# Performance work log

Hardware: AMD Instinct MI355X
Metric: run time of the kernel (lower is better)

Reference implementation:

```python
import jax, jax.numpy as jnp
import numpy as np

B, NQ, NC = 256, 15, 30          # pairs, query size, corpus size (= max_set_size)
EQ, EC = 45, 90                  # original directed edges per query / corpus graph
ENEW = NQ * (NC - NQ)            # edges added to pad each query graph
NPG = 2 * NC                     # nodes per pair after padding
N = B * NPG                      # 15360 total nodes
E = B * (EQ + EC + ENEW)         # 92160 total edges
D = 128                          # node_state_dim == filters_3
T = 64                           # transform_dim
N_PROP = 5
SK_ITERS, SK_TEMP = 10, 0.1


def _glorot(rng, shape):
    fan_in, fan_out = shape[0], shape[-1]
    s = np.sqrt(2.0 / (fan_in + fan_out))
    return jnp.asarray(rng.standard_normal(shape) * s, dtype=jnp.float32)


def setup_inputs() -> dict:
    rng = np.random.default_rng(0)
    frs, tos = [], []
    # original edges, grouped per pair as (query graph, corpus graph)
    for i in range(B):
        qoff, coff = i * NPG, i * NPG + NC
        frs.append(rng.integers(0, NQ, EQ) + qoff)
        tos.append(rng.integers(0, NQ, EQ) + qoff)
        frs.append(rng.integers(0, NC, EC) + coff)
        tos.append(rng.integers(0, NC, EC) + coff)
    # new padding edges: from each original query node to each new node
    for i in range(B):
        qoff = i * NPG
        frs.append(np.repeat(np.arange(NQ), NC - NQ) + qoff)
        tos.append(np.tile(np.arange(NQ, NC), NQ) + qoff)
    from_idx = jnp.asarray(np.concatenate(frs), dtype=jnp.int32)
    to_idx = jnp.asarray(np.concatenate(tos), dtype=jnp.int32)
    n_orig = B * (EQ + EC)
    mask_from_idx = jnp.concatenate([jnp.ones(n_orig), jnp.zeros(E - n_orig)]).astype(jnp.float32)
    inp = {
        'node_features': jnp.ones((N, 1), jnp.float32),
        'edge_features': jnp.ones((E, 1), jnp.float32),
        'mask_from_idx': mask_from_idx,
        'enc_node_w': _glorot(rng, (1, D)), 'enc_node_b': jnp.zeros(D, jnp.float32),
        'enc_edge_w': _glorot(rng, (1, D)), 'enc_edge_b': jnp.zeros(D, jnp.float32),
        'msg_w1': _glorot(rng, (3 * D, 2 * D)), 'msg_b1': jnp.zeros(2 * D, jnp.float32),
        'msg_w2': _glorot(rng, (2 * D, D)), 'msg_b2': jnp.zeros(D, jnp.float32),
        'upd_w1': _glorot(rng, (2 * D, 2 * D)), 'upd_b1': jnp.zeros(2 * D, jnp.float32),
        'upd_w2': _glorot(rng, (2 * D, D)), 'upd_b2': jnp.zeros(D, jnp.float32),
        'ft1_w': _glorot(rng, (D, T)), 'ft1_b': jnp.zeros(T, jnp.float32),
        'ft2_w': _glorot(rng, (T, T)), 'ft2_b': jnp.zeros(T, jnp.float32),
        'from_idx': from_idx, 'to_idx': to_idx,
    }
    return inp


def reference(node_features, edge_features, mask_from_idx,
              enc_node_w, enc_node_b, enc_edge_w, enc_edge_b,
              msg_w1, msg_b1, msg_w2, msg_b2,
              upd_w1, upd_b1, upd_w2, upd_b2,
              ft1_w, ft1_b, ft2_w, ft2_b,
              from_idx, to_idx):
    # GraphEncoder: linear embed of all-ones node/edge features
    h = node_features @ enc_node_w + enc_node_b          # [N, D]
    e = edge_features @ enc_edge_w + enc_edge_b          # [E, D]
    m = mask_from_idx[:, None]
    # shared GraphPropLayer applied n_prop_layers times
    for _ in range(N_PROP):
        msg_in = jnp.concatenate([h[from_idx], h[to_idx], e], axis=-1)      # [E, 3D]
        msg = jax.nn.relu(msg_in @ msg_w1 + msg_b1) @ msg_w2 + msg_b2       # [E, D]
        agg = jax.ops.segment_sum(msg * m, to_idx, num_segments=N)          # [N, D]
        upd_in = jnp.concatenate([agg, h], axis=-1)                          # [N, 2D]
        h = h + (jax.nn.relu(upd_in @ upd_w1 + upd_b1) @ upd_w2 + upd_b2)   # residual update
    hp = h.reshape(B, 2, NC, D)
    q_emb, c_emb = hp[:, 0], hp[:, 1]                    # [B, NC, D] each
    def transform(x):
        return jax.nn.relu(x @ ft1_w + ft1_b) @ ft2_w + ft2_b
    # query mask: only first NQ (original) nodes kept; corpus graphs are full size
    q_mask = (jnp.arange(NC) < NQ).astype(h.dtype)[None, :, None]
    tq = transform(q_emb) * q_mask                       # [B, NC, T]
    tc = transform(c_emb)                                # [B, NC, T]
    log_alpha = jnp.einsum('bqt,bct->bqc', tq, tc) / SK_TEMP
    for _ in range(SK_ITERS):
        log_alpha = log_alpha - jax.nn.logsumexp(log_alpha, axis=2, keepdims=True)
        log_alpha = log_alpha - jax.nn.logsumexp(log_alpha, axis=1, keepdims=True)
    tp = jnp.exp(log_alpha)                              # [B, NC, NC] transport plan
    moved = jnp.einsum('bqc,bcd->bqd', tp, c_emb)
    scores = -jnp.sum(jax.nn.relu(q_emb - moved), axis=(1, 2))  # [B]
    return scores
```

## Files before the change

### kernel.cpp

```cpp
#include <hip/hip_runtime.h>

#define BATCH 256
#define D 128
#define TT 64
#define NPG 60
#define NCC 30
#define NQQ 15
#define EPG 135
#define NPROP 5
#define SKI 10

typedef __attribute__((ext_vector_type(8))) short bf16x8;
typedef __attribute__((ext_vector_type(4))) float f32x4;

union U8 { bf16x8 v; uint4 u; };

__device__ __forceinline__ unsigned short f2bf(float f) {
    union { float f; unsigned int i; } t;
    t.f = f;
    unsigned int r = t.i + 0x7fffu + ((t.i >> 16) & 1u);
    return (unsigned short)(r >> 16);
}
__device__ __forceinline__ float bf2f(unsigned short u) {
    union { float f; unsigned int i; } t;
    t.i = ((unsigned int)u) << 16;
    return t.f;
}
__device__ __forceinline__ void split_bf(float v, unsigned short& hi, unsigned short& lo) {
    hi = f2bf(v);
    lo = f2bf(v - bf2f(hi));
}

__device__ __forceinline__ void splitv(float4 a, float4 b, bf16x8& hi, bf16x8& lo) {
    unsigned int ia0=__float_as_uint(a.x), ia1=__float_as_uint(a.y);
    unsigned int ia2=__float_as_uint(a.z), ia3=__float_as_uint(a.w);
    unsigned int ib0=__float_as_uint(b.x), ib1=__float_as_uint(b.y);
    unsigned int ib2=__float_as_uint(b.z), ib3=__float_as_uint(b.w);
    U8 uh, ul;
    uh.u = make_uint4((ia0>>16)|(ia1&0xffff0000u), (ia2>>16)|(ia3&0xffff0000u),
                      (ib0>>16)|(ib1&0xffff0000u), (ib2>>16)|(ib3&0xffff0000u));
    float r0 = a.x - __uint_as_float(ia0&0xffff0000u);
    float r1 = a.y - __uint_as_float(ia1&0xffff0000u);
    float r2 = a.z - __uint_as_float(ia2&0xffff0000u);
    float r3 = a.w - __uint_as_float(ia3&0xffff0000u);
    float r4 = b.x - __uint_as_float(ib0&0xffff0000u);
    float r5 = b.y - __uint_as_float(ib1&0xffff0000u);
    float r6 = b.z - __uint_as_float(ib2&0xffff0000u);
    float r7 = b.w - __uint_as_float(ib3&0xffff0000u);
    ul.u = make_uint4((__float_as_uint(r0)>>16)|(__float_as_uint(r1)&0xffff0000u),
                      (__float_as_uint(r2)>>16)|(__float_as_uint(r3)&0xffff0000u),
                      (__float_as_uint(r4)>>16)|(__float_as_uint(r5)&0xffff0000u),
                      (__float_as_uint(r6)>>16)|(__float_as_uint(r7)&0xffff0000u));
    hi = uh.v; lo = ul.v;
}

#define MFMA3(ah, al, bh, bl, acc)                                              \
    acc = __builtin_amdgcn_mfma_f32_16x16x32_bf16(ah, bh, acc, 0, 0, 0);        \
    acc = __builtin_amdgcn_mfma_f32_16x16x32_bf16(al, bh, acc, 0, 0, 0);        \
    acc = __builtin_amdgcn_mfma_f32_16x16x32_bf16(ah, bl, acc, 0, 0, 0);

__global__ void k_prep_uv(const float* __restrict__ ew, const float* __restrict__ eb,
                          const float* __restrict__ w1, const float* __restrict__ b1,
                          float* __restrict__ uv) {
    int t = threadIdx.x;
    float u = 0.f, v = 0.f;
    for (int d = 0; d < D; ++d) {
        float wv = w1[(256 + d) * 256 + t];
        u += ew[d] * wv;
        v += eb[d] * wv;
    }
    uv[t] = u;
    uv[256 + t] = v + b1[t];
}

__global__ void k_prep_w2(const float* __restrict__ mw1, const float* __restrict__ mw2,
                          const float* __restrict__ uw1, const float* __restrict__ uw2,
                          const float* __restrict__ f1w, const float* __restrict__ f2w,
                          unsigned short* __restrict__ w1h, unsigned short* __restrict__ w1l,
                          unsigned short* __restrict__ w2h, unsigned short* __restrict__ w2l,
                          unsigned short* __restrict__ u1h, unsigned short* __restrict__ u1l,
                          unsigned short* __restrict__ u2h, unsigned short* __restrict__ u2l,
                          unsigned short* __restrict__ g1h, unsigned short* __restrict__ g1l,
                          unsigned short* __restrict__ g2h, unsigned short* __restrict__ g2l) {
    int idx = blockIdx.x * 512 + threadIdx.x;
    int o, KS;
    unsigned short *ph, *pl;
    int mtype;
    if (idx < 65536)        { o = idx;          KS = 4; ph = w1h; pl = w1l; mtype = 0; }
    else if (idx < 98304)   { o = idx - 65536;  KS = 8; ph = w2h; pl = w2l; mtype = 1; }
    else if (idx < 163840)  { o = idx - 98304;  KS = 8; ph = u1h; pl = u1l; mtype = 2; }
    else if (idx < 196608)  { o = idx - 163840; KS = 8; ph = u2h; pl = u2l; mtype = 3; }
    else if (idx < 204800)  { o = idx - 196608; KS = 4; ph = g1h; pl = g1l; mtype = 4; }
    else if (idx < 208896)  { o = idx - 204800; KS = 2; ph = g2h; pl = g2l; mtype = 5; }
    else return;
    int t = o & 7;
    int l = (o >> 3) & 63;
    int frag = o >> 9;
    int ks = frag % KS;
    int nfr = frag / KS;
    int n = nfr * 16 + (l & 15);
    int k = ks * 32 + (l >> 4) * 8 + t;
    float v;
    switch (mtype) {
        case 0: v = (n < 256) ? mw1[k * 256 + n] : mw1[(128 + k) * 256 + (n - 256)]; break;
        case 1: v = mw2[k * 128 + n]; break;
        case 2: v = uw1[k * 256 + n]; break;
        case 3: v = uw2[k * 128 + n]; break;
        case 4: v = f1w[k * 64 + n]; break;
        default: v = f2w[k * 64 + n]; break;
    }
    unsigned short hi, lo;
    split_bf(v, hi, lo);
    ph[o] = hi;
    pl[o] = lo;
}

__global__ __launch_bounds__(512, 2) void k_mega(
    const float* __restrict__ nfeat, const float* __restrict__ efeat,
    const float* __restrict__ mfi,
    const float* __restrict__ enw, const float* __restrict__ enb,
    const float* __restrict__ uvg,
    const unsigned short* __restrict__ w1h, const unsigned short* __restrict__ w1l,
    const unsigned short* __restrict__ w2h, const unsigned short* __restrict__ w2l,
    const unsigned short* __restrict__ u1h, const unsigned short* __restrict__ u1l,
    const unsigned short* __restrict__ u2h, const unsigned short* __restrict__ u2l,
    const unsigned short* __restrict__ g1h, const unsigned short* __restrict__ g1l,
    const unsigned short* __restrict__ g2h, const unsigned short* __restrict__ g2l,
    const float* __restrict__ mb2, const float* __restrict__ ub1,
    const float* __restrict__ ub2, const float* __restrict__ f1b,
    const float* __restrict__ f2b,
    const int* __restrict__ fr, const int* __restrict__ to,
    float* __restrict__ out) {
    __shared__ __align__(16) float hS[60][132];
    __shared__ __align__(16) float H1S[45][516];
    __shared__ __align__(16) float aggS[45][132];
    __shared__ float uS[256], vS[256];
    __shared__ int cfS[144], ctS[144];
    __shared__ float efS[144], msS[144];
    __shared__ float b2S[128], ub1S[256], ub2S[128], f1bS[64], f2bS[64];

    int g = blockIdx.x;
    int tid = threadIdx.x;
    int wid = tid >> 6, lane = tid & 63;
    int l15 = lane & 15, l4 = lane >> 4;
    int rloc = l4 * 4;

    if (tid < 256) uS[tid] = uvg[tid];
    else vS[tid - 256] = uvg[tid];
    if (tid < 128) b2S[tid] = mb2[tid];
    if (tid < 256) ub1S[tid] = ub1[tid];
    if (tid < 128) ub2S[tid] = ub2[tid];
    if (tid < 64) { f1bS[tid] = f1b[tid]; f2bS[tid] = f2b[tid]; }
    if (tid < EPG) {
        int fn = fr[g * EPG + tid] - g * NPG;
        int tn = to[g * EPG + tid] - g * NPG;
        cfS[tid] = fn < 15 ? fn : fn - 15;
        ctS[tid] = tn < 15 ? tn : tn - 15;
        efS[tid] = efeat[g * EPG + tid];
        msS[tid] = mfi[g * EPG + tid];
    } else if (tid < 144) {
        cfS[tid] = 0; ctS[tid] = 0; efS[tid] = 0.f; msS[tid] = 0.f;
    }
    for (int i = tid; i < 60 * 128; i += 512) {
        int r = i >> 7, d = i & 127;
        hS[r][d] = nfeat[g * NPG + r] * enw[d] + enb[d];
    }
    __syncthreads();

    float* US = &H1S[0][0];
    char* zb = (char*)&aggS[0][0];

    for (int iter = 0; iter < NPROP; ++iter) {
        {
            f32x4 acc[3][4] = {};
#pragma unroll
            for (int ks = 0; ks < 4; ++ks) {
                int k0 = ks * 32 + l4 * 8;
                bf16x8 ah[3], al[3];
#pragma unroll
                for (int i = 0; i < 3; ++i) {
                    int r = i * 16 + l15;
                    int hr = r < 15 ? r : (r < 45 ? r + 15 : 0);
                    float4 a0 = *(const float4*)&hS[hr][k0];
                    float4 a1 = *(const float4*)&hS[hr][k0 + 4];
                    splitv(a0, a1, ah[i], al[i]);
                }
#pragma unroll
                for (int j = 0; j < 4; ++j) {
                    int nfr = wid * 4 + j;
                    int off = ((nfr * 4 + ks) * 64 + lane) * 8;
                    U8 th, tl;
                    th.u = *(const uint4*)(w1h + off);
                    tl.u = *(const uint4*)(w1l + off);
#pragma unroll
                    for (int i = 0; i < 3; ++i) { MFMA3(ah[i], al[i], th.v, tl.v, acc[i][j]); }
                }
            }
#pragma unroll
            for (int i = 0; i < 3; ++i)
#pragma unroll
                for (int j = 0; j < 4; ++j) {
                    int col = wid * 64 + j * 16 + l15;
#pragma unroll
                    for (int r = 0; r < 4; ++r) {
                        int m = i * 16 + rloc + r;
                        if (m < 45) H1S[m][col] = acc[i][j][r];
                    }
                }
        }
        __syncthreads();

        {
            f32x4 accB[9] = {};
#pragma unroll
            for (int ks = 0; ks < 8; ++ks) {
                __syncthreads();
                for (int u = tid; u < 576; u += 512) {
                    int f = u >> 6, l = u & 63;
                    int e = f * 16 + (l & 15);
                    int k0 = ks * 32 + (l >> 4) * 8;
                    int ee = e < EPG ? e : 0;
                    int cf = cfS[ee], ct = ctS[ee];
                    float ev = e < EPG ? efS[ee] : 0.f;
                    float4 x0 = *(const float4*)&H1S[cf][k0];
                    float4 x1 = *(const float4*)&H1S[cf][k0 + 4];
                    float4 y0 = *(const float4*)&H1S[ct][256 + k0];
                    float4 y1 = *(const float4*)&H1S[ct][256 + k0 + 4];
                    x0.x = fmaxf(x0.x + y0.x + ev * uS[k0 + 0] + vS[k0 + 0], 0.f);
                    x0.y = fmaxf(x0.y + y0.y + ev * uS[k0 + 1] + vS[k0 + 1], 0.f);
                    x0.z = fmaxf(x0.z + y0.z + ev * uS[k0 + 2] + vS[k0 + 2], 0.f);
                    x0.w = fmaxf(x0.w + y0.w + ev * uS[k0 + 3] + vS[k0 + 3], 0.f);
                    x1.x = fmaxf(x1.x + y1.x + ev * uS[k0 + 4] + vS[k0 + 4], 0.f);
                    x1.y = fmaxf(x1.y + y1.y + ev * uS[k0 + 5] + vS[k0 + 5], 0.f);
                    x1.z = fmaxf(x1.z + y1.z + ev * uS[k0 + 6] + vS[k0 + 6], 0.f);
                    x1.w = fmaxf(x1.w + y1.w + ev * uS[k0 + 7] + vS[k0 + 7], 0.f);
                    bf16x8 zh, zl;
                    splitv(x0, x1, zh, zl);
                    U8 sh, sl; sh.v = zh; sl.v = zl;
                    *(uint4*)(zb + f * 2048 + l * 16) = sh.u;
                    *(uint4*)(zb + f * 2048 + 1024 + l * 16) = sl.u;
                }
                __syncthreads();
                int off = ((wid * 8 + ks) * 64 + lane) * 8;
                U8 th, tl;
                th.u = *(const uint4*)(w2h + off);
                tl.u = *(const uint4*)(w2l + off);
#pragma unroll
                for (int f = 0; f < 9; ++f) {
                    bf16x8 zh = *(bf16x8*)(zb + f * 2048 + lane * 16);
                    bf16x8 zl = *(bf16x8*)(zb + f * 2048 + 1024 + lane * 16);
                    MFMA3(zh, zl, th.v, tl.v, accB[f]);
                }
            }
            __syncthreads();
            for (int i = tid; i < 45 * 132; i += 512) (&aggS[0][0])[i] = 0.f;
            __syncthreads();
            {
                int col = wid * 16 + l15;
                float bias = b2S[col];
#pragma unroll
                for (int f = 0; f < 9; ++f)
#pragma unroll
                    for (int r = 0; r < 4; ++r) {
                        int e = f * 16 + rloc + r;
                        if (e < EPG)
                            atomicAdd(&aggS[ctS[e]][col], (accB[f][r] + bias) * msS[e]);
                    }
            }
        }
        __syncthreads();

        {
            f32x4 accC[4][2] = {};
#pragma unroll
            for (int ks = 0; ks < 8; ++ks) {
                int k0 = ks * 32 + l4 * 8;
                bf16x8 bh[2], bl[2];
#pragma unroll
                for (int j = 0; j < 2; ++j) {
                    int nfr = wid * 2 + j;
                    int off = ((nfr * 8 + ks) * 64 + lane) * 8;
                    U8 th, tl;
                    th.u = *(const uint4*)(u1h + off);
                    tl.u = *(const uint4*)(u1l + off);
                    bh[j] = th.v; bl[j] = tl.v;
                }
#pragma unroll
                for (int mf = 0; mf < 4; ++mf) {
                    int p = mf * 16 + l15;
                    float4 z0, z1;
                    if (ks < 4) {
                        int ar = p < 15 ? p : (p < 60 ? p - 15 : 0);
                        z0 = *(const float4*)&aggS[ar][k0];
                        z1 = *(const float4*)&aggS[ar][k0 + 4];
                        float msk = (p >= 15 && p < 30) ? 0.f : 1.f;
                        z0.x *= msk; z0.y *= msk; z0.z *= msk; z0.w *= msk;
                        z1.x *= msk; z1.y *= msk; z1.z *= msk; z1.w *= msk;
                    } else {
                        int hr = p < 60 ? p : 0;
                        z0 = *(const float4*)&hS[hr][k0 - 128];
                        z1 = *(const float4*)&hS[hr][k0 - 128 + 4];
                    }
                    bf16x8 ah, al;
                    splitv(z0, z1, ah, al);
#pragma unroll
                    for (int j = 0; j < 2; ++j) { MFMA3(ah, al, bh[j], bl[j], accC[mf][j]); }
                }
            }
            __syncthreads();
#pragma unroll
            for (int mf = 0; mf < 4; ++mf)
#pragma unroll
                for (int j = 0; j < 2; ++j) {
                    int col = (wid * 2 + j) * 16 + l15;
                    float bias = ub1S[col];
#pragma unroll
                    for (int r = 0; r < 4; ++r) {
                        int m = mf * 16 + rloc + r;
                        if (m < 60) US[m * 260 + col] = fmaxf(accC[mf][j][r] + bias, 0.f);
                    }
                }
        }
        __syncthreads();

        {
            f32x4 accD[4] = {};
#pragma unroll
            for (int ks = 0; ks < 8; ++ks) {
                int k0 = ks * 32 + l4 * 8;
                int off = ((wid * 8 + ks) * 64 + lane) * 8;
                U8 th, tl;
                th.u = *(const uint4*)(u2h + off);
                tl.u = *(const uint4*)(u2l + off);
#pragma unroll
                for (int mf = 0; mf < 4; ++mf) {
                    int p = mf * 16 + l15;
                    int pr = p < 60 ? p : 0;
                    float4 z0 = *(const float4*)&US[pr * 260 + k0];
                    float4 z1 = *(const float4*)&US[pr * 260 + k0 + 4];
                    bf16x8 ah, al;
                    splitv(z0, z1, ah, al);
                    MFMA3(ah, al, th.v, tl.v, accD[mf]);
                }
            }
#pragma unroll
            for (int mf = 0; mf < 4; ++mf) {
                int col = wid * 16 + l15;
                float bias = ub2S[col];
#pragma unroll
                for (int r = 0; r < 4; ++r) {
                    int m = mf * 16 + rloc + r;
                    if (m < 60) hS[m][col] += accD[mf][r] + bias;
                }
            }
        }
        __syncthreads();
    }

    float* hid = &H1S[0][0];
    float* tS = hid + 45 * 68;
    float* la = &aggS[0][0];
    float* red = la + 1024;

    if (wid < 6) {
        int mf = wid >> 1, nh = wid & 1;
        f32x4 acc[2] = {};
#pragma unroll
        for (int ks = 0; ks < 4; ++ks) {
            int k0 = ks * 32 + l4 * 8;
            int r = mf * 16 + l15;
            int hr = r < 15 ? r : (r < 45 ? r + 15 : 0);
            float4 a0 = *(const float4*)&hS[hr][k0];
            float4 a1 = *(const float4*)&hS[hr][k0 + 4];
            bf16x8 ah, al;
            splitv(a0, a1, ah, al);
#pragma unroll
            for (int j = 0; j < 2; ++j) {
                int nfr = nh * 2 + j;
                int off = ((nfr * 4 + ks) * 64 + lane) * 8;
                U8 th, tl;
                th.u = *(const uint4*)(g1h + off);
                tl.u = *(const uint4*)(g1l + off);
                MFMA3(ah, al, th.v, tl.v, acc[j]);
            }
        }
#pragma unroll
        for (int j = 0; j < 2; ++j) {
            int col = nh * 32 + j * 16 + l15;
            float bias = f1bS[col];
#pragma unroll
            for (int r = 0; r < 4; ++r) {
                int m = mf * 16 + rloc + r;
                if (m < 45) hid[m * 68 + col] = fmaxf(acc[j][r] + bias, 0.f);
            }
        }
    }
    __syncthreads();
    if (wid < 6) {
        int mf = wid >> 1, nh = wid & 1;
        f32x4 acc[2] = {};
#pragma unroll
        for (int ks = 0; ks < 2; ++ks) {
            int k0 = ks * 32 + l4 * 8;
            int r = mf * 16 + l15;
            int hr = r < 45 ? r : 0;
            float4 a0 = *(const float4*)&hid[hr * 68 + k0];
            float4 a1 = *(const float4*)&hid[hr * 68 + k0 + 4];
            bf16x8 ah, al;
            splitv(a0, a1, ah, al);
#pragma unroll
            for (int j = 0; j < 2; ++j) {
                int nfr = nh * 2 + j;
                int off = ((nfr * 2 + ks) * 64 + lane) * 8;
                U8 th, tl;
                th.u = *(const uint4*)(g2h + off);
                tl.u = *(const uint4*)(g2l + off);
                MFMA3(ah, al, th.v, tl.v, acc[j]);
            }
        }
#pragma unroll
        for (int j = 0; j < 2; ++j) {
            int col = nh * 32 + j * 16 + l15;
            float bias = f2bS[col];
#pragma unroll
            for (int r = 0; r < 4; ++r) {
                int m = mf * 16 + rloc + r;
                if (m < 45) tS[m * 68 + col] = acc[j][r] + bias;
            }
        }
    }
    __syncthreads();
    for (int e = tid; e < NCC * NCC; e += 512) {
        int q = e / NCC, c = e % NCC;
        float s = 0.f;
        if (q < NQQ) {
#pragma unroll 4
            for (int k = 0; k < TT; k++) s += tS[q * 68 + k] * tS[(15 + c) * 68 + k];
            s *= 10.0f;
        }
        la[q * 33 + c] = s;
    }
    __syncthreads();
    int grp = tid >> 3, k8 = tid & 7;
    for (int it = 0; it < SKI; ++it) {
        if (grp < NCC) {
            float v0, v1, v2, v3, m;
            int c0 = k8 * 4;
            v0 = (c0 + 0 < NCC) ? la[grp * 33 + c0 + 0] : -INFINITY;
            v1 = (c0 + 1 < NCC) ? la[grp * 33 + c0 + 1] : -INFINITY;
            v2 = (c0 + 2 < NCC) ? la[grp * 33 + c0 + 2] : -INFINITY;
            v3 = (c0 + 3 < NCC) ? la[grp * 33 + c0 + 3] : -INFINITY;
            m = fmaxf(fmaxf(v0, v1), fmaxf(v2, v3));
            m = fmaxf(m, __shfl_xor(m, 1));
            m = fmaxf(m, __shfl_xor(m, 2));
            m = fmaxf(m, __shfl_xor(m, 4));
            float s = 0.f;
            if (c0 + 0 < NCC) s += __expf(v0 - m);
            if (c0 + 1 < NCC) s += __expf(v1 - m);
            if (c0 + 2 < NCC) s += __expf(v2 - m);
            if (c0 + 3 < NCC) s += __expf(v3 - m);
            s += __shfl_xor(s, 1);
            s += __shfl_xor(s, 2);
            s += __shfl_xor(s, 4);
            float lse = m + __logf(s);
            if (c0 + 0 < NCC) la[grp * 33 + c0 + 0] = v0 - lse;
            if (c0 + 1 < NCC) la[grp * 33 + c0 + 1] = v1 - lse;
            if (c0 + 2 < NCC) la[grp * 33 + c0 + 2] = v2 - lse;
            if (c0 + 3 < NCC) la[grp * 33 + c0 + 3] = v3 - lse;
        }
        __syncthreads();
        if (grp < NCC) {
            float v0, v1, v2, v3, m;
            int q0 = k8 * 4;
            v0 = (q0 + 0 < NCC) ? la[(q0 + 0) * 33 + grp] : -INFINITY;
            v1 = (q0 + 1 < NCC) ? la[(q0 + 1) * 33 + grp] : -INFINITY;
            v2 = (q0 + 2 < NCC) ? la[(q0 + 2) * 33 + grp] : -INFINITY;
            v3 = (q0 + 3 < NCC) ? la[(q0 + 3) * 33 + grp] : -INFINITY;
            m = fmaxf(fmaxf(v0, v1), fmaxf(v2, v3));
            m = fmaxf(m, __shfl_xor(m, 1));
            m = fmaxf(m, __shfl_xor(m, 2));
            m = fmaxf(m, __shfl_xor(m, 4));
            float s = 0.f;
            if (q0 + 0 < NCC) s += __expf(v0 - m);
            if (q0 + 1 < NCC) s += __expf(v1 - m);
            if (q0 + 2 < NCC) s += __expf(v2 - m);
            if (q0 + 3 < NCC) s += __expf(v3 - m);
            s += __shfl_xor(s, 1);
            s += __shfl_xor(s, 2);
            s += __shfl_xor(s, 4);
            float lse = m + __logf(s);
            if (q0 + 0 < NCC) la[(q0 + 0) * 33 + grp] = v0 - lse;
            if (q0 + 1 < NCC) la[(q0 + 1) * 33 + grp] = v1 - lse;
            if (q0 + 2 < NCC) la[(q0 + 2) * 33 + grp] = v2 - lse;
            if (q0 + 3 < NCC) la[(q0 + 3) * 33 + grp] = v3 - lse;
        }
        __syncthreads();
    }
    for (int e = tid; e < NCC * NCC; e += 512) {
        int q = e / NCC, c = e % NCC;
        la[q * 33 + c] = __expf(la[q * 33 + c]);
    }
    __syncthreads();
    float part = 0.f;
    for (int idx = tid; idx < NCC * D; idx += 512) {
        int q = idx >> 7, d = idx & 127;
        float mv = 0.f;
#pragma unroll 5
        for (int c = 0; c < NCC; c++) mv += la[q * 33 + c] * hS[30 + c][d];
        part += fmaxf(hS[q][d] - mv, 0.f);
    }
    red[tid] = part;
    __syncthreads();
    for (int s2 = 256; s2 > 0; s2 >>= 1) {
        if (tid < s2) red[tid] += red[tid + s2];
        __syncthreads();
    }
    if (tid == 0) out[g] = -red[0];
}

extern "C" void kernel_launch(void* const* d_in, const int* in_sizes, int n_in,
                              void* d_out, int out_size, void* d_ws, size_t ws_size,
                              hipStream_t stream) {
    const float* nf  = (const float*)d_in[0];
    const float* ef  = (const float*)d_in[1];
    const float* mfi = (const float*)d_in[2];
    const float* enw = (const float*)d_in[3];
    const float* enb = (const float*)d_in[4];
    const float* eew = (const float*)d_in[5];
    const float* eeb = (const float*)d_in[6];
    const float* mw1 = (const float*)d_in[7];
    const float* mb1 = (const float*)d_in[8];
    const float* mw2 = (const float*)d_in[9];
    const float* mb2 = (const float*)d_in[10];
    const float* uw1 = (const float*)d_in[11];
    const float* ub1 = (const float*)d_in[12];
    const float* uw2 = (const float*)d_in[13];
    const float* ub2 = (const float*)d_in[14];
    const float* f1w = (const float*)d_in[15];
    const float* f1b = (const float*)d_in[16];
    const float* f2w = (const float*)d_in[17];
    const float* f2b = (const float*)d_in[18];
    const int* fr = (const int*)d_in[19];
    const int* to = (const int*)d_in[20];
    float* out = (float*)d_out;

    char* base = (char*)d_ws;
    float* uv = (float*)base;
    unsigned short* w = (unsigned short*)(base + 4096);
    unsigned short* w1h = w;            unsigned short* w1l = w1h + 65536;
    unsigned short* w2h = w1l + 65536;  unsigned short* w2l = w2h + 32768;
    unsigned short* u1h = w2l + 32768;  unsigned short* u1l = u1h + 65536;
    unsigned short* u2h = u1l + 65536;  unsigned short* u2l = u2h + 32768;
    unsigned short* g1h = u2l + 32768;  unsigned short* g1l = g1h + 8192;
    unsigned short* g2h = g1l + 8192;   unsigned short* g2l = g2h + 4096;

    k_prep_uv<<<1, 256, 0, stream>>>(eew, eeb, mw1, mb1, uv);
    k_prep_w2<<<408, 512, 0, stream>>>(mw1, mw2, uw1, uw2, f1w, f2w,
                                       w1h, w1l, w2h, w2l, u1h, u1l, u2h, u2l,
                                       g1h, g1l, g2h, g2l);
    k_mega<<<BATCH, 512, 0, stream>>>(nf, ef, mfi, enw, enb, uv,
                                      w1h, w1l, w2h, w2l, u1h, u1l, u2h, u2l,
                                      g1h, g1l, g2h, g2l,
                                      mb2, ub1, ub2, f1b, f2b, fr, to, out);
}
```

Measured before the change: 371.2 us.

## Compute message MLP per edge directly and store node states pre-split to cut LDS

The node state is now kept in shared memory as packed bf16 hi/lo pairs, so MFMA operands are unpacked instead of re-split each time. The message first layer now runs on gathered per-edge inputs, in chunks fused with the second layer, instead of precomputing per-node halves into a large H1 buffer. The update MLP is fused the same way through a small staging buffer. Shared memory drops enough that launch bounds move from 2 to 4 blocks per CU, trading more MFMA work per edge for occupancy.

```diff
diff --git a/kernel.cpp b/kernel.cpp
--- a/kernel.cpp
+++ b/kernel.cpp
@@ -21,16 +21,24 @@
     unsigned int r = t.i + 0x7fffu + ((t.i >> 16) & 1u);
     return (unsigned short)(r >> 16);
 }
-__device__ __forceinline__ float bf2f(unsigned short u) {
-    union { float f; unsigned int i; } t;
-    t.i = ((unsigned int)u) << 16;
-    return t.f;
-}
-__device__ __forceinline__ void split_bf(float v, unsigned short& hi, unsigned short& lo) {
-    hi = f2bf(v);
-    lo = f2bf(v - bf2f(hi));
-}
-
+__device__ __forceinline__ unsigned int pkv(float v) {
+    unsigned int ih = __float_as_uint(v) & 0xffff0000u;
+    float r = v - __uint_as_float(ih);
+    return ih | (__float_as_uint(r) >> 16);
+}
+__device__ __forceinline__ float upkv(unsigned int p) {
+    return __uint_as_float(p & 0xffff0000u) + __uint_as_float(p << 16);
+}
+__device__ __forceinline__ void unpack8(const unsigned int* s, bf16x8& hi, bf16x8& lo) {
+    uint4 a = *(const uint4*)s;
+    uint4 b = *(const uint4*)(s + 4);
+    U8 h, l;
+    h.u = make_uint4((a.x >> 16) | (a.y & 0xffff0000u), (a.z >> 16) | (a.w & 0xffff0000u),
+                     (b.x >> 16) | (b.y & 0xffff0000u), (b.z >> 16) | (b.w & 0xffff0000u));
+    l.u = make_uint4((a.x & 0xffffu) | (a.y << 16), (a.z & 0xffffu) | (a.w << 16),
+                     (b.x & 0xffffu) | (b.y << 16), (b.z & 0xffffu) | (b.w << 16));
+    hi = h.v; lo = l.v;
+}
 __device__ __forceinline__ void splitv(float4 a, float4 b, bf16x8& hi, bf16x8& lo) {
     unsigned int ia0=__float_as_uint(a.x), ia1=__float_as_uint(a.y);
     unsigned int ia2=__float_as_uint(a.z), ia3=__float_as_uint(a.w);
@@ -53,6 +61,11 @@
                       (__float_as_uint(r6)>>16)|(__float_as_uint(r7)&0xffff0000u));
     hi = uh.v; lo = ul.v;
 }
+__device__ __forceinline__ void split_bf(float v, unsigned short& hi, unsigned short& lo) {
+    hi = f2bf(v);
+    union { float f; unsigned int i; } t; t.i = ((unsigned int)hi) << 16;
+    lo = f2bf(v - t.f);
+}
 
 #define MFMA3(ah, al, bh, bl, acc)                                              \
     acc = __builtin_amdgcn_mfma_f32_16x16x32_bf16(ah, bh, acc, 0, 0, 0);        \
@@ -86,7 +99,7 @@
     int o, KS;
     unsigned short *ph, *pl;
     int mtype;
-    if (idx < 65536)        { o = idx;          KS = 4; ph = w1h; pl = w1l; mtype = 0; }
+    if (idx < 65536)        { o = idx;          KS = 8; ph = w1h; pl = w1l; mtype = 0; }
     else if (idx < 98304)   { o = idx - 65536;  KS = 8; ph = w2h; pl = w2l; mtype = 1; }
     else if (idx < 163840)  { o = idx - 98304;  KS = 8; ph = u1h; pl = u1l; mtype = 2; }
     else if (idx < 196608)  { o = idx - 163840; KS = 8; ph = u2h; pl = u2l; mtype = 3; }
@@ -102,7 +115,7 @@
     int k = ks * 32 + (l >> 4) * 8 + t;
     float v;
     switch (mtype) {
-        case 0: v = (n < 256) ? mw1[k * 256 + n] : mw1[(128 + k) * 256 + (n - 256)]; break;
+        case 0: v = mw1[k * 256 + n]; break;
         case 1: v = mw2[k * 128 + n]; break;
         case 2: v = uw1[k * 256 + n]; break;
         case 3: v = uw2[k * 128 + n]; break;
@@ -115,7 +128,7 @@
     pl[o] = lo;
 }
 
-__global__ __launch_bounds__(512, 2) void k_mega(
+__global__ __launch_bounds__(512, 4) void k_mega(
     const float* __restrict__ nfeat, const float* __restrict__ efeat,
     const float* __restrict__ mfi,
     const float* __restrict__ enw, const float* __restrict__ enb,
@@ -131,236 +144,198 @@
     const float* __restrict__ f2b,
     const int* __restrict__ fr, const int* __restrict__ to,
     float* __restrict__ out) {
-    __shared__ __align__(16) float hS[60][132];
-    __shared__ __align__(16) float H1S[45][516];
-    __shared__ __align__(16) float aggS[45][132];
+    __shared__ __align__(16) unsigned int hSp[60][132];
+    __shared__ __align__(16) char pool[42240];
     __shared__ float uS[256], vS[256];
-    __shared__ int cfS[144], ctS[144];
+    __shared__ int cfS[144], ctRawS[144], ctCmpS[144];
     __shared__ float efS[144], msS[144];
-    __shared__ float b2S[128], ub1S[256], ub2S[128], f1bS[64], f2bS[64];
-
-    int g = blockIdx.x;
-    int tid = threadIdx.x;
+
+    float* aggS = (float*)pool;
+    char* zb = pool + 23760;
+
+    int g = blockIdx.x, tid = threadIdx.x;
     int wid = tid >> 6, lane = tid & 63;
-    int l15 = lane & 15, l4 = lane >> 4;
-    int rloc = l4 * 4;
+    int l15 = lane & 15, l4 = lane >> 4, rloc = l4 * 4;
 
     if (tid < 256) uS[tid] = uvg[tid];
     else vS[tid - 256] = uvg[tid];
-    if (tid < 128) b2S[tid] = mb2[tid];
-    if (tid < 256) ub1S[tid] = ub1[tid];
-    if (tid < 128) ub2S[tid] = ub2[tid];
-    if (tid < 64) { f1bS[tid] = f1b[tid]; f2bS[tid] = f2b[tid]; }
-    if (tid < EPG) {
-        int fn = fr[g * EPG + tid] - g * NPG;
-        int tn = to[g * EPG + tid] - g * NPG;
-        cfS[tid] = fn < 15 ? fn : fn - 15;
-        ctS[tid] = tn < 15 ? tn : tn - 15;
-        efS[tid] = efeat[g * EPG + tid];
-        msS[tid] = mfi[g * EPG + tid];
-    } else if (tid < 144) {
-        cfS[tid] = 0; ctS[tid] = 0; efS[tid] = 0.f; msS[tid] = 0.f;
+    if (tid < 144) {
+        if (tid < EPG) {
+            int fn = fr[g * EPG + tid] - g * NPG;
+            int tn = to[g * EPG + tid] - g * NPG;
+            cfS[tid] = fn;
+            ctRawS[tid] = tn;
+            ctCmpS[tid] = tn < 15 ? tn : tn - 15;
+            efS[tid] = efeat[g * EPG + tid];
+            msS[tid] = mfi[g * EPG + tid];
+        } else {
+            cfS[tid] = 0; ctRawS[tid] = 0; ctCmpS[tid] = 0; efS[tid] = 0.f; msS[tid] = 0.f;
+        }
     }
     for (int i = tid; i < 60 * 128; i += 512) {
         int r = i >> 7, d = i & 127;
-        hS[r][d] = nfeat[g * NPG + r] * enw[d] + enb[d];
+        hSp[r][d] = pkv(nfeat[g * NPG + r] * enw[d] + enb[d]);
     }
     __syncthreads();
 
-    float* US = &H1S[0][0];
-    char* zb = (char*)&aggS[0][0];
+    float biasB = mb2[wid * 16 + l15];
+    float biasD = ub2[wid * 16 + l15];
 
     for (int iter = 0; iter < NPROP; ++iter) {
+        for (int i = tid; i < 45 * 132; i += 512) aggS[i] = 0.f;
+
+        f32x4 accB[9] = {};
+        for (int c = 0; c < 8; ++c) {
+            __syncthreads();
+            U8 wbh, wbl;
+            {
+                int off = ((wid * 8 + c) * 64 + lane) * 8;
+                wbh.u = *(const uint4*)(w2h + off);
+                wbl.u = *(const uint4*)(w2l + off);
+            }
+            f32x4 az[2][2] = {};
+#pragma unroll
+            for (int kk = 0; kk < 8; ++kk) {
+                int kloc = (kk & 3) * 32 + l4 * 8;
+                bf16x8 ah0, al0, ah1, al1;
+                {
+                    int e = wid * 16 + l15;
+                    int row = (kk < 4) ? cfS[e] : ctRawS[e];
+                    unpack8(&hSp[row][kloc], ah0, al0);
+                }
+                if (wid == 0) {
+                    int e = 128 + l15;
+                    int row = (kk < 4) ? cfS[e] : ctRawS[e];
+                    unpack8(&hSp[row][kloc], ah1, al1);
+                }
+#pragma unroll
+                for (int nf = 0; nf < 2; ++nf) {
+                    int off = (((c * 2 + nf) * 8 + kk) * 64 + lane) * 8;
+                    U8 bh, bl;
+                    bh.u = *(const uint4*)(w1h + off);
+                    bl.u = *(const uint4*)(w1l + off);
+                    MFMA3(ah0, al0, bh.v, bl.v, az[0][nf]);
+                    if (wid == 0) { MFMA3(ah1, al1, bh.v, bl.v, az[1][nf]); }
+                }
+            }
+#pragma unroll
+            for (int mi = 0; mi < 2; ++mi) {
+                if (mi == 1 && wid != 0) continue;
+                int mf = (mi == 0) ? wid : 8;
+#pragma unroll
+                for (int nf = 0; nf < 2; ++nf) {
+                    int kj = nf * 16 + l15;
+                    int ncol = c * 32 + kj;
+                    float uvn = uS[ncol], vvn = vS[ncol];
+#pragma unroll
+                    for (int r = 0; r < 4; ++r) {
+                        int e = mf * 16 + rloc + r;
+                        float val = fmaxf(az[mi][nf][r] + efS[e] * uvn + vvn, 0.f);
+                        unsigned int p = pkv(val);
+                        int base = mf * 2048 + (kj >> 3) * 256 + (rloc + r) * 16 + (kj & 7) * 2;
+                        *(unsigned short*)(zb + base) = (unsigned short)(p >> 16);
+                        *(unsigned short*)(zb + base + 1024) = (unsigned short)(p & 0xffffu);
+                    }
+                }
+            }
+            __syncthreads();
+#pragma unroll
+            for (int f = 0; f < 9; ++f) {
+                bf16x8 zh = *(bf16x8*)(zb + f * 2048 + lane * 16);
+                bf16x8 zl = *(bf16x8*)(zb + f * 2048 + 1024 + lane * 16);
+                MFMA3(zh, zl, wbh.v, wbl.v, accB[f]);
+            }
+        }
+        __syncthreads();
         {
-            f32x4 acc[3][4] = {};
-#pragma unroll
-            for (int ks = 0; ks < 4; ++ks) {
-                int k0 = ks * 32 + l4 * 8;
-                bf16x8 ah[3], al[3];
-#pragma unroll
-                for (int i = 0; i < 3; ++i) {
-                    int r = i * 16 + l15;
-                    int hr = r < 15 ? r : (r < 45 ? r + 15 : 0);
-                    float4 a0 = *(const float4*)&hS[hr][k0];
-                    float4 a1 = *(const float4*)&hS[hr][k0 + 4];
-                    splitv(a0, a1, ah[i], al[i]);
-                }
-#pragma unroll
-                for (int j = 0; j < 4; ++j) {
-                    int nfr = wid * 4 + j;
-                    int off = ((nfr * 4 + ks) * 64 + lane) * 8;
-                    U8 th, tl;
-                    th.u = *(const uint4*)(w1h + off);
-                    tl.u = *(const uint4*)(w1l + off);
-#pragma unroll
-                    for (int i = 0; i < 3; ++i) { MFMA3(ah[i], al[i], th.v, tl.v, acc[i][j]); }
-                }
-            }
-#pragma unroll
-            for (int i = 0; i < 3; ++i)
-#pragma unroll
-                for (int j = 0; j < 4; ++j) {
-                    int col = wid * 64 + j * 16 + l15;
-#pragma unroll
-                    for (int r = 0; r < 4; ++r) {
-                        int m = i * 16 + rloc + r;
-                        if (m < 45) H1S[m][col] = acc[i][j][r];
+            int col = wid * 16 + l15;
+#pragma unroll
+            for (int f = 0; f < 9; ++f)
+#pragma unroll
+                for (int r = 0; r < 4; ++r) {
+                    int e = f * 16 + rloc + r;
+                    if (e < EPG)
+                        atomicAdd(&aggS[ctCmpS[e] * 132 + col], (accB[f][r] + biasB) * msS[e]);
+                }
+        }
+        __syncthreads();
+
+        f32x4 accD[4] = {};
+        int mfc = wid >> 1, nfc = wid & 1;
+        int pC = mfc * 16 + l15;
+        int arC = pC < 15 ? pC : (pC < 60 ? pC - 15 : 0);
+        float mskC = ((pC >= 15 && pC < 30) || pC >= 60) ? 0.f : 1.f;
+        int hrC = pC < 60 ? pC : 0;
+        for (int c = 0; c < 8; ++c) {
+            __syncthreads();
+            U8 wdh, wdl;
+            {
+                int off = ((wid * 8 + c) * 64 + lane) * 8;
+                wdh.u = *(const uint4*)(u2h + off);
+                wdl.u = *(const uint4*)(u2l + off);
+            }
+            f32x4 au = {};
+#pragma unroll
+            for (int kk = 0; kk < 8; ++kk) {
+                bf16x8 ah, al;
+                if (kk < 4) {
+                    int k0 = kk * 32 + l4 * 8;
+                    float4 z0 = *(const float4*)&aggS[arC * 132 + k0];
+                    float4 z1 = *(const float4*)&aggS[arC * 132 + k0 + 4];
+                    z0.x *= mskC; z0.y *= mskC; z0.z *= mskC; z0.w *= mskC;
+                    z1.x *= mskC; z1.y *= mskC; z1.z *= mskC; z1.w *= mskC;
+                    splitv(z0, z1, ah, al);
+                } else {
+                    int k0 = (kk - 4) * 32 + l4 * 8;
+                    unpack8(&hSp[hrC][k0], ah, al);
+                }
+                int off = (((c * 2 + nfc) * 8 + kk) * 64 + lane) * 8;
+                U8 bh, bl;
+                bh.u = *(const uint4*)(u1h + off);
+                bl.u = *(const uint4*)(u1l + off);
+                MFMA3(ah, al, bh.v, bl.v, au);
+            }
+            {
+                int kj = nfc * 16 + l15;
+                float b1v = ub1[c * 32 + kj];
+#pragma unroll
+                for (int r = 0; r < 4; ++r) {
+                    float val = fmaxf(au[r] + b1v, 0.f);
+                    unsigned int p = pkv(val);
+                    int base = mfc * 2048 + (kj >> 3) * 256 + (rloc + r) * 16 + (kj & 7) * 2;
+                    *(unsigned short*)(zb + base) = (unsigned short)(p >> 16);
+                    *(unsigned short*)(zb + base + 1024) = (unsigned short)(p & 0xffffu);
+                }
+            }
+            __syncthreads();
+#pragma unroll
+            for (int f = 0; f < 4; ++f) {
+                bf16x8 zh = *(bf16x8*)(zb + f * 2048 + lane * 16);
+                bf16x8 zl = *(bf16x8*)(zb + f * 2048 + 1024 + lane * 16);
+                MFMA3(zh, zl, wdh.v, wdl.v, accD[f]);
+            }
+        }
+        __syncthreads();
+        {
+            int col = wid * 16 + l15;
+#pragma unroll
+            for (int f = 0; f < 4; ++f)
+#pragma unroll
+                for (int r = 0; r < 4; ++r) {
+                    int m = f * 16 + rloc + r;
+                    if (m < 60) {
+                        float v = upkv(hSp[m][col]) + accD[f][r] + biasD;
+                        hSp[m][col] = pkv(v);
                     }
                 }
         }
         __syncthreads();
-
-        {
-            f32x4 accB[9] = {};
-#pragma unroll
-            for (int ks = 0; ks < 8; ++ks) {
-                __syncthreads();
-                for (int u = tid; u < 576; u += 512) {
-                    int f = u >> 6, l = u & 63;
-                    int e = f * 16 + (l & 15);
-                    int k0 = ks * 32 + (l >> 4) * 8;
-                    int ee = e < EPG ? e : 0;
-                    int cf = cfS[ee], ct = ctS[ee];
-                    float ev = e < EPG ? efS[ee] : 0.f;
-                    float4 x0 = *(const float4*)&H1S[cf][k0];
-                    float4 x1 = *(const float4*)&H1S[cf][k0 + 4];
-                    float4 y0 = *(const float4*)&H1S[ct][256 + k0];
-                    float4 y1 = *(const float4*)&H1S[ct][256 + k0 + 4];
-                    x0.x = fmaxf(x0.x + y0.x + ev * uS[k0 + 0] + vS[k0 + 0], 0.f);
-                    x0.y = fmaxf(x0.y + y0.y + ev * uS[k0 + 1] + vS[k0 + 1], 0.f);
-                    x0.z = fmaxf(x0.z + y0.z + ev * uS[k0 + 2] + vS[k0 + 2], 0.f);
-                    x0.w = fmaxf(x0.w + y0.w + ev * uS[k0 + 3] + vS[k0 + 3], 0.f);
-                    x1.x = fmaxf(x1.x + y1.x + ev * uS[k0 + 4] + vS[k0 + 4], 0.f);
-                    x1.y = fmaxf(x1.y + y1.y + ev * uS[k0 + 5] + vS[k0 + 5], 0.f);
-                    x1.z = fmaxf(x1.z + y1.z + ev * uS[k0 + 6] + vS[k0 + 6], 0.f);
-                    x1.w = fmaxf(x1.w + y1.w + ev * uS[k0 + 7] + vS[k0 + 7], 0.f);
-                    bf16x8 zh, zl;
-                    splitv(x0, x1, zh, zl);
-                    U8 sh, sl; sh.v = zh; sl.v = zl;
-                    *(uint4*)(zb + f * 2048 + l * 16) = sh.u;
-                    *(uint4*)(zb + f * 2048 + 1024 + l * 16) = sl.u;
-                }
-                __syncthreads();
-                int off = ((wid * 8 + ks) * 64 + lane) * 8;
-                U8 th, tl;
-                th.u = *(const uint4*)(w2h + off);
-                tl.u = *(const uint4*)(w2l + off);
-#pragma unroll
-                for (int f = 0; f < 9; ++f) {
-                    bf16x8 zh = *(bf16x8*)(zb + f * 2048 + lane * 16);
-                    bf16x8 zl = *(bf16x8*)(zb + f * 2048 + 1024 + lane * 16);
-                    MFMA3(zh, zl, th.v, tl.v, accB[f]);
-                }
-            }
-            __syncthreads();
-            for (int i = tid; i < 45 * 132; i += 512) (&aggS[0][0])[i] = 0.f;
-            __syncthreads();
-            {
-                int col = wid * 16 + l15;
-                float bias = b2S[col];
-#pragma unroll
-                for (int f = 0; f < 9; ++f)
-#pragma unroll
-                    for (int r = 0; r < 4; ++r) {
-                        int e = f * 16 + rloc + r;
-                        if (e < EPG)
-                            atomicAdd(&aggS[ctS[e]][col], (accB[f][r] + bias) * msS[e]);
-                    }
-            }
-        }
-        __syncthreads();
-
-        {
-            f32x4 accC[4][2] = {};
-#pragma unroll
-            for (int ks = 0; ks < 8; ++ks) {
-                int k0 = ks * 32 + l4 * 8;
-                bf16x8 bh[2], bl[2];
-#pragma unroll
-                for (int j = 0; j < 2; ++j) {
-                    int nfr = wid * 2 + j;
-                    int off = ((nfr * 8 + ks) * 64 + lane) * 8;
-                    U8 th, tl;
-                    th.u = *(const uint4*)(u1h + off);
-                    tl.u = *(const uint4*)(u1l + off);
-                    bh[j] = th.v; bl[j] = tl.v;
-                }
-#pragma unroll
-                for (int mf = 0; mf < 4; ++mf) {
-                    int p = mf * 16 + l15;
-                    float4 z0, z1;
-                    if (ks < 4) {
-                        int ar = p < 15 ? p : (p < 60 ? p - 15 : 0);
-                        z0 = *(const float4*)&aggS[ar][k0];
-                        z1 = *(const float4*)&aggS[ar][k0 + 4];
-                        float msk = (p >= 15 && p < 30) ? 0.f : 1.f;
-                        z0.x *= msk; z0.y *= msk; z0.z *= msk; z0.w *= msk;
-                        z1.x *= msk; z1.y *= msk; z1.z *= msk; z1.w *= msk;
-                    } else {
-                        int hr = p < 60 ? p : 0;
-                        z0 = *(const float4*)&hS[hr][k0 - 128];
-                        z1 = *(const float4*)&hS[hr][k0 - 128 + 4];
-                    }
-                    bf16x8 ah, al;
-                    splitv(z0, z1, ah, al);
-#pragma unroll
-                    for (int j = 0; j < 2; ++j) { MFMA3(ah, al, bh[j], bl[j], accC[mf][j]); }
-                }
-            }
-            __syncthreads();
-#pragma unroll
-            for (int mf = 0; mf < 4; ++mf)
-#pragma unroll
-                for (int j = 0; j < 2; ++j) {
-                    int col = (wid * 2 + j) * 16 + l15;
-                    float bias = ub1S[col];
-#pragma unroll
-                    for (int r = 0; r < 4; ++r) {
-                        int m = mf * 16 + rloc + r;
-                        if (m < 60) US[m * 260 + col] = fmaxf(accC[mf][j][r] + bias, 0.f);
-                    }
-                }
-        }
-        __syncthreads();
-
-        {
-            f32x4 accD[4] = {};
-#pragma unroll
-            for (int ks = 0; ks < 8; ++ks) {
-                int k0 = ks * 32 + l4 * 8;
-                int off = ((wid * 8 + ks) * 64 + lane) * 8;
-                U8 th, tl;
-                th.u = *(const uint4*)(u2h + off);
-                tl.u = *(const uint4*)(u2l + off);
-#pragma unroll
-                for (int mf = 0; mf < 4; ++mf) {
-                    int p = mf * 16 + l15;
-                    int pr = p < 60 ? p : 0;
-                    float4 z0 = *(const float4*)&US[pr * 260 + k0];
-                    float4 z1 = *(const float4*)&US[pr * 260 + k0 + 4];
-                    bf16x8 ah, al;
-                    splitv(z0, z1, ah, al);
-                    MFMA3(ah, al, th.v, tl.v, accD[mf]);
-                }
-            }
-#pragma unroll
-            for (int mf = 0; mf < 4; ++mf) {
-                int col = wid * 16 + l15;
-                float bias = ub2S[col];
-#pragma unroll
-                for (int r = 0; r < 4; ++r) {
-                    int m = mf * 16 + rloc + r;
-                    if (m < 60) hS[m][col] += accD[mf][r] + bias;
-                }
-            }
-        }
-        __syncthreads();
-    }
-
-    float* hid = &H1S[0][0];
+    }
+
+    float* hid = (float*)pool;
     float* tS = hid + 45 * 68;
-    float* la = &aggS[0][0];
-    float* red = la + 1024;
+    float* la = tS + 45 * 68;
+    float* red = la + 30 * 33;
 
     if (wid < 6) {
         int mf = wid >> 1, nh = wid & 1;
@@ -370,10 +345,8 @@
             int k0 = ks * 32 + l4 * 8;
             int r = mf * 16 + l15;
             int hr = r < 15 ? r : (r < 45 ? r + 15 : 0);
-            float4 a0 = *(const float4*)&hS[hr][k0];
-            float4 a1 = *(const float4*)&hS[hr][k0 + 4];
             bf16x8 ah, al;
-            splitv(a0, a1, ah, al);
+            unpack8(&hSp[hr][k0], ah, al);
 #pragma unroll
             for (int j = 0; j < 2; ++j) {
                 int nfr = nh * 2 + j;
@@ -387,7 +360,7 @@
 #pragma unroll
         for (int j = 0; j < 2; ++j) {
             int col = nh * 32 + j * 16 + l15;
-            float bias = f1bS[col];
+            float bias = f1b[col];
 #pragma unroll
             for (int r = 0; r < 4; ++r) {
                 int m = mf * 16 + rloc + r;
@@ -421,7 +394,7 @@
 #pragma unroll
         for (int j = 0; j < 2; ++j) {
             int col = nh * 32 + j * 16 + l15;
-            float bias = f2bS[col];
+            float bias = f2b[col];
 #pragma unroll
             for (int r = 0; r < 4; ++r) {
                 int m = mf * 16 + rloc + r;
@@ -506,8 +479,8 @@
         int q = idx >> 7, d = idx & 127;
         float mv = 0.f;
 #pragma unroll 5
-        for (int c = 0; c < NCC; c++) mv += la[q * 33 + c] * hS[30 + c][d];
-        part += fmaxf(hS[q][d] - mv, 0.f);
+        for (int c = 0; c < NCC; c++) mv += la[q * 33 + c] * upkv(hSp[30 + c][d]);
+        part += fmaxf(upkv(hSp[q][d]) - mv, 0.f);
     }
     red[tid] = part;
     __syncthreads();
```

Result: slower. 507.4 us (+36.7%).

## Widen mega-kernel to 768 threads and redistribute GEMM tiles across twelve waves

Applied to the files above, without the earlier changes.

Raises the block size from 512 to 768 threads (12 waves, launch bounds one block per CU). Each GEMM stage's tiling is repartitioned: the first message GEMM is split by row fragment and column group, the edge GEMM by edge-fragment group and column pair, and the update GEMMs loop over column or tile indices strided by the wave count. The aim is more in-flight waves per CU to hide LDS and MFMA latency, since only 256 blocks are launched. The trade-offs are uneven tile counts across waves in the update stages, fewer registers available per thread, and a reduction buffer that must now hold 1024 entries.

```diff
diff --git a/kernel.cpp b/kernel.cpp
--- a/kernel.cpp
+++ b/kernel.cpp
@@ -9,6 +9,7 @@
 #define EPG 135
 #define NPROP 5
 #define SKI 10
+#define NT 768
 
 typedef __attribute__((ext_vector_type(8))) short bf16x8;
 typedef __attribute__((ext_vector_type(4))) float f32x4;
@@ -115,7 +116,7 @@
     pl[o] = lo;
 }
 
-__global__ __launch_bounds__(512, 2) void k_mega(
+__global__ __launch_bounds__(NT, 1) void k_mega(
     const float* __restrict__ nfeat, const float* __restrict__ efeat,
     const float* __restrict__ mfi,
     const float* __restrict__ enw, const float* __restrict__ enb,
@@ -146,7 +147,7 @@
     int rloc = l4 * 4;
 
     if (tid < 256) uS[tid] = uvg[tid];
-    else vS[tid - 256] = uvg[tid];
+    else if (tid < 512) vS[tid - 256] = uvg[tid];
     if (tid < 128) b2S[tid] = mb2[tid];
     if (tid < 256) ub1S[tid] = ub1[tid];
     if (tid < 128) ub2S[tid] = ub2[tid];
@@ -161,7 +162,7 @@
     } else if (tid < 144) {
         cfS[tid] = 0; ctS[tid] = 0; efS[tid] = 0.f; msS[tid] = 0.f;
     }
-    for (int i = tid; i < 60 * 128; i += 512) {
+    for (int i = tid; i < 60 * 128; i += NT) {
         int r = i >> 7, d = i & 127;
         hS[r][d] = nfeat[g * NPG + r] * enw[d] + enb[d];
     }
@@ -172,51 +173,58 @@
 
     for (int iter = 0; iter < NPROP; ++iter) {
         {
-            f32x4 acc[3][4] = {};
+            int mfa = wid >> 2;
+            int nfb = wid & 3;
+            f32x4 acc[8] = {};
 #pragma unroll
             for (int ks = 0; ks < 4; ++ks) {
                 int k0 = ks * 32 + l4 * 8;
-                bf16x8 ah[3], al[3];
-#pragma unroll
-                for (int i = 0; i < 3; ++i) {
-                    int r = i * 16 + l15;
-                    int hr = r < 15 ? r : (r < 45 ? r + 15 : 0);
-                    float4 a0 = *(const float4*)&hS[hr][k0];
-                    float4 a1 = *(const float4*)&hS[hr][k0 + 4];
-                    splitv(a0, a1, ah[i], al[i]);
-                }
-#pragma unroll
-                for (int j = 0; j < 4; ++j) {
-                    int nfr = wid * 4 + j;
+                int r = mfa * 16 + l15;
+                int hr = r < 15 ? r : (r < 45 ? r + 15 : 0);
+                float4 a0 = *(const float4*)&hS[hr][k0];
+                float4 a1 = *(const float4*)&hS[hr][k0 + 4];
+                bf16x8 ah, al;
+                splitv(a0, a1, ah, al);
+#pragma unroll
+                for (int j = 0; j < 8; ++j) {
+                    int nfr = nfb + j * 4;
                     int off = ((nfr * 4 + ks) * 64 + lane) * 8;
                     U8 th, tl;
                     th.u = *(const uint4*)(w1h + off);
                     tl.u = *(const uint4*)(w1l + off);
-#pragma unroll
-                    for (int i = 0; i < 3; ++i) { MFMA3(ah[i], al[i], th.v, tl.v, acc[i][j]); }
-                }
-            }
-#pragma unroll
-            for (int i = 0; i < 3; ++i)
-#pragma unroll
-                for (int j = 0; j < 4; ++j) {
-                    int col = wid * 64 + j * 16 + l15;
-#pragma unroll
-                    for (int r = 0; r < 4; ++r) {
-                        int m = i * 16 + rloc + r;
-                        if (m < 45) H1S[m][col] = acc[i][j][r];
-                    }
-                }
+                    MFMA3(ah, al, th.v, tl.v, acc[j]);
+                }
+            }
+#pragma unroll
+            for (int j = 0; j < 8; ++j) {
+                int col = (nfb + j * 4) * 16 + l15;
+#pragma unroll
+                for (int r = 0; r < 4; ++r) {
+                    int m = mfa * 16 + rloc + r;
+                    if (m < 45) H1S[m][col] = acc[j][r];
+                }
+            }
         }
         __syncthreads();
 
         {
-            f32x4 accB[9] = {};
+            int nfp = wid & 3;
+            int ft3 = (wid >> 2) * 3;
+            f32x4 accB[3][2] = {};
 #pragma unroll
             for (int ks = 0; ks < 8; ++ks) {
                 __syncthreads();
-                for (int u = tid; u < 576; u += 512) {
-                    int f = u >> 6, l = u & 63;
+                U8 wh0, wl0, wh1, wl1;
+                {
+                    int off0 = (((2 * nfp) * 8 + ks) * 64 + lane) * 8;
+                    int off1 = (((2 * nfp + 1) * 8 + ks) * 64 + lane) * 8;
+                    wh0.u = *(const uint4*)(w2h + off0);
+                    wl0.u = *(const uint4*)(w2l + off0);
+                    wh1.u = *(const uint4*)(w2h + off1);
+                    wl1.u = *(const uint4*)(w2l + off1);
+                }
+                if (tid < 576) {
+                    int f = tid >> 6, l = tid & 63;
                     int e = f * 16 + (l & 15);
                     int k0 = ks * 32 + (l >> 4) * 8;
                     int ee = e < EPG ? e : 0;
@@ -241,116 +249,109 @@
                     *(uint4*)(zb + f * 2048 + 1024 + l * 16) = sl.u;
                 }
                 __syncthreads();
-                int off = ((wid * 8 + ks) * 64 + lane) * 8;
-                U8 th, tl;
-                th.u = *(const uint4*)(w2h + off);
-                tl.u = *(const uint4*)(w2l + off);
-#pragma unroll
-                for (int f = 0; f < 9; ++f) {
+#pragma unroll
+                for (int fi = 0; fi < 3; ++fi) {
+                    int f = ft3 + fi;
                     bf16x8 zh = *(bf16x8*)(zb + f * 2048 + lane * 16);
                     bf16x8 zl = *(bf16x8*)(zb + f * 2048 + 1024 + lane * 16);
-                    MFMA3(zh, zl, th.v, tl.v, accB[f]);
+                    MFMA3(zh, zl, wh0.v, wl0.v, accB[fi][0]);
+                    MFMA3(zh, zl, wh1.v, wl1.v, accB[fi][1]);
                 }
             }
             __syncthreads();
-            for (int i = tid; i < 45 * 132; i += 512) (&aggS[0][0])[i] = 0.f;
+            for (int i = tid; i < 45 * 132; i += NT) (&aggS[0][0])[i] = 0.f;
             __syncthreads();
-            {
-                int col = wid * 16 + l15;
+#pragma unroll
+            for (int jj = 0; jj < 2; ++jj) {
+                int col = (2 * nfp + jj) * 16 + l15;
                 float bias = b2S[col];
 #pragma unroll
-                for (int f = 0; f < 9; ++f)
+                for (int fi = 0; fi < 3; ++fi)
 #pragma unroll
                     for (int r = 0; r < 4; ++r) {
-                        int e = f * 16 + rloc + r;
+                        int e = (ft3 + fi) * 16 + rloc + r;
                         if (e < EPG)
-                            atomicAdd(&aggS[ctS[e]][col], (accB[f][r] + bias) * msS[e]);
+                            atomicAdd(&aggS[ctS[e]][col], (accB[fi][jj][r] + bias) * msS[e]);
                     }
             }
         }
         __syncthreads();
 
         {
-            f32x4 accC[4][2] = {};
-#pragma unroll
-            for (int ks = 0; ks < 8; ++ks) {
-                int k0 = ks * 32 + l4 * 8;
-                bf16x8 bh[2], bl[2];
-#pragma unroll
-                for (int j = 0; j < 2; ++j) {
-                    int nfr = wid * 2 + j;
-                    int off = ((nfr * 8 + ks) * 64 + lane) * 8;
+            for (int nfc = wid; nfc < 16; nfc += 12) {
+                bf16x8 CH[8], CL[8];
+#pragma unroll
+                for (int ks = 0; ks < 8; ++ks) {
+                    int off = ((nfc * 8 + ks) * 64 + lane) * 8;
                     U8 th, tl;
                     th.u = *(const uint4*)(u1h + off);
                     tl.u = *(const uint4*)(u1l + off);
-                    bh[j] = th.v; bl[j] = tl.v;
+                    CH[ks] = th.v; CL[ks] = tl.v;
+                }
+                f32x4 accC[4] = {};
+#pragma unroll
+                for (int ks = 0; ks < 8; ++ks) {
+                    int k0 = ks * 32 + l4 * 8;
+#pragma unroll
+                    for (int mf = 0; mf < 4; ++mf) {
+                        int p = mf * 16 + l15;
+                        float4 z0, z1;
+                        if (ks < 4) {
+                            int ar = p < 15 ? p : (p < 60 ? p - 15 : 0);
+                            z0 = *(const float4*)&aggS[ar][k0];
+                            z1 = *(const float4*)&aggS[ar][k0 + 4];
+                            float msk = (p >= 15 && p < 30) ? 0.f : 1.f;
+                            z0.x *= msk; z0.y *= msk; z0.z *= msk; z0.w *= msk;
+                            z1.x *= msk; z1.y *= msk; z1.z *= msk; z1.w *= msk;
+                        } else {
+                            int hr = p < 60 ? p : 0;
+                            z0 = *(const float4*)&hS[hr][k0 - 128];
+                            z1 = *(const float4*)&hS[hr][k0 - 128 + 4];
+                        }
+                        bf16x8 ah, al;
+                        splitv(z0, z1, ah, al);
+                        MFMA3(ah, al, CH[ks], CL[ks], accC[mf]);
+                    }
                 }
 #pragma unroll
                 for (int mf = 0; mf < 4; ++mf) {
-                    int p = mf * 16 + l15;
-                    float4 z0, z1;
-                    if (ks < 4) {
-                        int ar = p < 15 ? p : (p < 60 ? p - 15 : 0);
-                        z0 = *(const float4*)&aggS[ar][k0];
-                        z1 = *(const float4*)&aggS[ar][k0 + 4];
-                        float msk = (p >= 15 && p < 30) ? 0.f : 1.f;
-                        z0.x *= msk; z0.y *= msk; z0.z *= msk; z0.w *= msk;
-                        z1.x *= msk; z1.y *= msk; z1.z *= msk; z1.w *= msk;
-                    } else {
-                        int hr = p < 60 ? p : 0;
-                        z0 = *(const float4*)&hS[hr][k0 - 128];
-                        z1 = *(const float4*)&hS[hr][k0 - 128 + 4];
-                    }
-                    bf16x8 ah, al;
-                    splitv(z0, z1, ah, al);
-#pragma unroll
-                    for (int j = 0; j < 2; ++j) { MFMA3(ah, al, bh[j], bl[j], accC[mf][j]); }
-                }
-            }
-            __syncthreads();
-#pragma unroll
-            for (int mf = 0; mf < 4; ++mf)
-#pragma unroll
-                for (int j = 0; j < 2; ++j) {
-                    int col = (wid * 2 + j) * 16 + l15;
+                    int col = nfc * 16 + l15;
                     float bias = ub1S[col];
 #pragma unroll
                     for (int r = 0; r < 4; ++r) {
                         int m = mf * 16 + rloc + r;
-                        if (m < 60) US[m * 260 + col] = fmaxf(accC[mf][j][r] + bias, 0.f);
+                        if (m < 60) US[m * 260 + col] = fmaxf(accC[mf][r] + bias, 0.f);
                     }
                 }
+            }
         }
         __syncthreads();
 
         {
-            f32x4 accD[4] = {};
-#pragma unroll
-            for (int ks = 0; ks < 8; ++ks) {
-                int k0 = ks * 32 + l4 * 8;
-                int off = ((wid * 8 + ks) * 64 + lane) * 8;
-                U8 th, tl;
-                th.u = *(const uint4*)(u2h + off);
-                tl.u = *(const uint4*)(u2l + off);
-#pragma unroll
-                for (int mf = 0; mf < 4; ++mf) {
+            for (int t = wid; t < 32; t += 12) {
+                int mf = t >> 3, nfd = t & 7;
+                f32x4 accD = {};
+#pragma unroll
+                for (int ks = 0; ks < 8; ++ks) {
+                    int k0 = ks * 32 + l4 * 8;
+                    int off = ((nfd * 8 + ks) * 64 + lane) * 8;
+                    U8 th, tl;
+                    th.u = *(const uint4*)(u2h + off);
+                    tl.u = *(const uint4*)(u2l + off);
                     int p = mf * 16 + l15;
                     int pr = p < 60 ? p : 0;
                     float4 z0 = *(const float4*)&US[pr * 260 + k0];
                     float4 z1 = *(const float4*)&US[pr * 260 + k0 + 4];
                     bf16x8 ah, al;
                     splitv(z0, z1, ah, al);
-                    MFMA3(ah, al, th.v, tl.v, accD[mf]);
-                }
-            }
-#pragma unroll
-            for (int mf = 0; mf < 4; ++mf) {
-                int col = wid * 16 + l15;
+                    MFMA3(ah, al, th.v, tl.v, accD);
+                }
+                int col = nfd * 16 + l15;
                 float bias = ub2S[col];
 #pragma unroll
                 for (int r = 0; r < 4; ++r) {
                     int m = mf * 16 + rloc + r;
-                    if (m < 60) hS[m][col] += accD[mf][r] + bias;
+                    if (m < 60) hS[m][col] += accD[r] + bias;
                 }
             }
         }
@@ -430,7 +431,7 @@
         }
     }
     __syncthreads();
-    for (int e = tid; e < NCC * NCC; e += 512) {
+    for (int e = tid; e < NCC * NCC; e += NT) {
         int q = e / NCC, c = e % NCC;
         float s = 0.f;
         if (q < NQQ) {
@@ -496,13 +497,13 @@
         }
         __syncthreads();
     }
-    for (int e = tid; e < NCC * NCC; e += 512) {
+    for (int e = tid; e < NCC * NCC; e += NT) {
         int q = e / NCC, c = e % NCC;
         la[q * 33 + c] = __expf(la[q * 33 + c]);
     }
     __syncthreads();
     float part = 0.f;
-    for (int idx = tid; idx < NCC * D; idx += 512) {
+    for (int idx = tid; idx < NCC * D; idx += NT) {
         int q = idx >> 7, d = idx & 127;
         float mv = 0.f;
 #pragma unroll 5
@@ -510,8 +511,9 @@
         part += fmaxf(hS[q][d] - mv, 0.f);
     }
     red[tid] = part;
+    if (tid < 1024 - NT) red[NT + tid] = 0.f;
     __syncthreads();
-    for (int s2 = 256; s2 > 0; s2 >>= 1) {
+    for (int s2 = 512; s2 > 0; s2 >>= 1) {
         if (tid < s2) red[tid] += red[tid + s2];
         __syncthreads();
     }
@@ -558,8 +560,8 @@
     k_prep_w2<<<408, 512, 0, stream>>>(mw1, mw2, uw1, uw2, f1w, f2w,
                                        w1h, w1l, w2h, w2l, u1h, u1l, u2h, u2l,
                                        g1h, g1l, g2h, g2l);
-    k_mega<<<BATCH, 512, 0, stream>>>(nf, ef, mfi, enw, enb, uv,
-                                      w1h, w1l, w2h, w2l, u1h, u1l, u2h, u2l,
-                                      g1h, g1l, g2h, g2l,
-                                      mb2, ub1, ub2, f1b, f2b, fr, to, out);
-}
+    k_mega<<<BATCH, NT, 0, stream>>>(nf, ef, mfi, enw, enb, uv,
+                                     w1h, w1l, w2h, w2l, u1h, u1l, u2h, u2l,
+                                     g1h, g1l, g2h, g2l,
+                                     mb2, ub1, ub2, f1b, f2b, fr, to, out);
+}
```

Result: slower. 1.043 ms (+181.0%).
